# Kernel tuning notes

Hardware: AMD Instinct MI355X
Metric: run time of the kernel (lower is better)

The kernel has to match this reference:

```python
import jax, jax.numpy as jnp
import numpy as np

H, W = 480, 640          # sensor resolution (self.dim)
N = 16_777_216           # number of events


def setup_inputs() -> dict:
    key = jax.random.key(0)
    k1, k2, k3, k4 = jax.random.split(key, 4)
    x = jax.random.randint(k1, (N,), 0, W).astype(jnp.float32)
    y = jax.random.randint(k2, (N,), 0, H).astype(jnp.float32)
    t = jax.random.uniform(k3, (N,), minval=1e-3, maxval=1.0)
    p = jax.random.randint(k4, (N,), 0, 2).astype(jnp.float32) * 2.0 - 1.0  # {-1, +1}
    events = jnp.stack([x, y, t, p], axis=1)  # [N, 4]
    return {"events": events}


def reference(events):
    # events: [N, 4] columns (x, y, t, p)
    x, y, t, p = events.T
    t = t / t.max()          # computed in original (unused for indexing)
    p = (p + 1.0) / 2.0      # {-1,1} -> {0,1}
    idx = (x + W * y + W * H * p).astype(jnp.int32)  # [N] flat voxel index
    # scatter-add event counts, then binarize (vox_ec[vox_ec > 0] = 1)
    vox = jnp.zeros(2 * H * W, dtype=events.dtype).at[idx].add(jnp.ones_like(x))
    vox = jnp.where(vox > 0, jnp.ones_like(vox), vox)
    return vox.reshape(-1, 2, H, W)  # [1, 2, H, W]
```

## Files before the change

kernel.cpp:

```cpp
#include <hip/hip_runtime.h>
#include <hip/hip_bf16.h>

#define HW_W 640
#define HW_H 480

typedef float vf4 __attribute__((ext_vector_type(4)));

__global__ void __launch_bounds__(256)
event_scatter_kernel(const vf4* __restrict__ events,
                     float* __restrict__ out, int n) {
    int i = blockIdx.x * blockDim.x + threadIdx.x;
    if (i < n) {
        vf4 e = __builtin_nontemporal_load(events + i);
        float p01 = (e.w + 1.0f) * 0.5f;
        int idx = (int)(e.x + (float)HW_W * e.y + (float)(HW_W * HW_H) * p01);
        out[idx] = 1.0f;
    }
}

extern "C" void kernel_launch(void* const* d_in, const int* in_sizes, int n_in,
                              void* d_out, int out_size, void* d_ws, size_t ws_size,
                              hipStream_t stream) {
    const vf4* events = (const vf4*)d_in[0];
    float* out = (float*)d_out;
    int n = in_sizes[0] / 4;

    hipMemsetAsync(d_out, 0, (size_t)out_size * sizeof(float), stream);

    int block = 256;
    int grid = (n + block - 1) / block;
    event_scatter_kernel<<<grid, block, 0, stream>>>(events, out, n);
}
```

Before: 433.9 us.

## Build per-block LDS bitmap with atomicOr, merge globally, then expand to floats

Replaces random global float stores with shared-memory bitmap atomics per block, merged into a global bitmap in the workspace and expanded into the dense float output by a second kernel. This removes scattered global writes and the full-output memset. In exchange it adds a large LDS footprint that limits occupancy, per-block global atomic merges, and an extra kernel launch.

Result: faster. 372.4 us (-14.2%).

```diff
diff --git a/kernel.cpp b/kernel.cpp
--- a/kernel.cpp
+++ b/kernel.cpp
@@ -1,20 +1,58 @@
 #include <hip/hip_runtime.h>
 #include <hip/hip_bf16.h>
 
-#define HW_W 640
-#define HW_H 480
+#define EW 640
+#define EH 480
+#define NVOX (2 * EH * EW)
+#define NWORDS (NVOX / 32)
+#define BLK 512
 
 typedef float vf4 __attribute__((ext_vector_type(4)));
 
+__device__ __forceinline__ int ev_idx(vf4 e) {
+    float p01 = (e.w + 1.0f) * 0.5f;
+    return (int)(e.x + (float)EW * e.y + (float)(EW * EH) * p01);
+}
+
+__global__ void __launch_bounds__(BLK, 4)
+event_bitmap_kernel(const vf4* __restrict__ events,
+                    unsigned int* __restrict__ gbm, int n) {
+    __shared__ unsigned int bm[NWORDS];
+    for (int w = threadIdx.x; w < NWORDS; w += BLK) bm[w] = 0u;
+    __syncthreads();
+
+    const int nth = gridDim.x * BLK;
+    int i = blockIdx.x * BLK + threadIdx.x;
+    for (; i + 3 * nth < n; i += 4 * nth) {
+        vf4 e0 = events[i];
+        vf4 e1 = events[i + nth];
+        vf4 e2 = events[i + 2 * nth];
+        vf4 e3 = events[i + 3 * nth];
+        int x0 = ev_idx(e0), x1 = ev_idx(e1), x2 = ev_idx(e2), x3 = ev_idx(e3);
+        atomicOr(&bm[x0 >> 5], 1u << (x0 & 31));
+        atomicOr(&bm[x1 >> 5], 1u << (x1 & 31));
+        atomicOr(&bm[x2 >> 5], 1u << (x2 & 31));
+        atomicOr(&bm[x3 >> 5], 1u << (x3 & 31));
+    }
+    for (; i < n; i += nth) {
+        vf4 e = events[i];
+        int x = ev_idx(e);
+        atomicOr(&bm[x >> 5], 1u << (x & 31));
+    }
+    __syncthreads();
+
+    for (int w = threadIdx.x; w < NWORDS; w += BLK) {
+        unsigned int v = bm[w];
+        if (v) atomicOr(&gbm[w], v);
+    }
+}
+
 __global__ void __launch_bounds__(256)
-event_scatter_kernel(const vf4* __restrict__ events,
-                     float* __restrict__ out, int n) {
-    int i = blockIdx.x * blockDim.x + threadIdx.x;
-    if (i < n) {
-        vf4 e = __builtin_nontemporal_load(events + i);
-        float p01 = (e.w + 1.0f) * 0.5f;
-        int idx = (int)(e.x + (float)HW_W * e.y + (float)(HW_W * HW_H) * p01);
-        out[idx] = 1.0f;
+expand_kernel(const unsigned int* __restrict__ gbm, float* __restrict__ out) {
+    int i = blockIdx.x * 256 + threadIdx.x;
+    if (i < NVOX) {
+        unsigned int wv = gbm[i >> 5];
+        out[i] = ((wv >> (i & 31)) & 1u) ? 1.0f : 0.0f;
     }
 }
 
@@ -22,12 +60,12 @@
                               void* d_out, int out_size, void* d_ws, size_t ws_size,
                               hipStream_t stream) {
     const vf4* events = (const vf4*)d_in[0];
+    unsigned int* gbm = (unsigned int*)d_ws;
     float* out = (float*)d_out;
     int n = in_sizes[0] / 4;
 
-    hipMemsetAsync(d_out, 0, (size_t)out_size * sizeof(float), stream);
+    hipMemsetAsync(gbm, 0, NWORDS * sizeof(unsigned int), stream);
 
-    int block = 256;
-    int grid = (n + block - 1) / block;
-    event_scatter_kernel<<<grid, block, 0, stream>>>(events, out, n);
+    event_bitmap_kernel<<<512, BLK, 0, stream>>>(events, gbm, n);
+    expand_kernel<<<(NVOX + 255) / 256, 256, 0, stream>>>(gbm, out);
 }
```

## Scatter events into global bitmap with atomicOr, then expand to floats

Applied to the files above, without the earlier changes.

Instead of writing 1.0f directly to the float voxel grid, each event sets a bit in a compact 19200-word global bitmap with atomicOr. A second kernel expands the bitmap into the float output with vectorized stores. The memset shrinks to the bitmap size. The cost is 16M atomics contending on a small array, where the old version used plain stores, plus an extra kernel launch.

New measurement: 1.042 ms. 2.4x slower.

```diff
diff --git a/kernel.cpp b/kernel.cpp
--- a/kernel.cpp
+++ b/kernel.cpp
@@ -1,20 +1,49 @@
 #include <hip/hip_runtime.h>
 #include <hip/hip_bf16.h>
 
-#define HW_W 640
-#define HW_H 480
+#define EW 640
+#define EH 480
+#define NVOX (2 * EH * EW)
+#define NWORDS (NVOX / 32)
+#define NCHUNK 16
 
 typedef float vf4 __attribute__((ext_vector_type(4)));
 
+__device__ __forceinline__ int ev_idx(vf4 e) {
+    float p01 = (e.w + 1.0f) * 0.5f;
+    return (int)(e.x + (float)EW * e.y + (float)(EW * EH) * p01);
+}
+
 __global__ void __launch_bounds__(256)
-event_scatter_kernel(const vf4* __restrict__ events,
-                     float* __restrict__ out, int n) {
-    int i = blockIdx.x * blockDim.x + threadIdx.x;
+event_atomic_kernel(const vf4* __restrict__ events,
+                    unsigned int* __restrict__ gbm, int n) {
+    int i = blockIdx.x * 256 + threadIdx.x;
     if (i < n) {
-        vf4 e = __builtin_nontemporal_load(events + i);
-        float p01 = (e.w + 1.0f) * 0.5f;
-        int idx = (int)(e.x + (float)HW_W * e.y + (float)(HW_W * HW_H) * p01);
-        out[idx] = 1.0f;
+        vf4 e = events[i];
+        int x = ev_idx(e);
+        atomicOr(&gbm[x >> 5], 1u << (x & 31));
+    }
+}
+
+__global__ void __launch_bounds__(256)
+expand_kernel(const unsigned int* __restrict__ gbm, float* __restrict__ out) {
+    __shared__ unsigned int sbm[256];
+    int w = blockIdx.x * 256 + threadIdx.x;
+    sbm[threadIdx.x] = gbm[w];
+    __syncthreads();
+
+    vf4* out4 = (vf4*)out + (size_t)blockIdx.x * 2048;
+    #pragma unroll
+    for (int q = 0; q < 8; ++q) {
+        int f = q * 256 + threadIdx.x;
+        unsigned int wv = sbm[f >> 3];
+        int sh = (f & 7) * 4;
+        vf4 v;
+        v.x = (wv >> (sh + 0)) & 1u ? 1.0f : 0.0f;
+        v.y = (wv >> (sh + 1)) & 1u ? 1.0f : 0.0f;
+        v.z = (wv >> (sh + 2)) & 1u ? 1.0f : 0.0f;
+        v.w = (wv >> (sh + 3)) & 1u ? 1.0f : 0.0f;
+        out4[f] = v;
     }
 }
 
@@ -25,9 +54,10 @@
     float* out = (float*)d_out;
     int n = in_sizes[0] / 4;
 
-    hipMemsetAsync(d_out, 0, (size_t)out_size * sizeof(float), stream);
+    unsigned int* gbm = (unsigned int*)d_ws;
 
-    int block = 256;
-    int grid = (n + block - 1) / block;
-    event_scatter_kernel<<<grid, block, 0, stream>>>(events, out, n);
+    hipMemsetAsync(gbm, 0, NWORDS * sizeof(unsigned int), stream);
+
+    event_atomic_kernel<<<(n + 255) / 256, 256, 0, stream>>>(events, gbm, n);
+    expand_kernel<<<NWORDS / 256, 256, 0, stream>>>(gbm, out);
 }
```
